# Optimization experiments

Measured on AMD Instinct MI355X. Metric: run time of the kernel, lower is better.

## Reference

```python
import jax, jax.numpy as jnp
import numpy as np

BATCH, SEQ, NUM_SUB, CB_SIZE, SUB_DIM = 8, 2048, 16, 1024, 64
EMB_DIM = NUM_SUB * SUB_DIM  # 1024


def setup_inputs() -> dict:
    key = jax.random.key(0)
    k1, k2 = jax.random.split(key)
    embeddings = jax.random.normal(k1, (BATCH, SEQ, EMB_DIM), dtype=jnp.float32)
    # stacked PQ codebooks: [num_subspaces, codebook_size, subspace_dim]
    codebooks = jax.random.normal(k2, (NUM_SUB, CB_SIZE, SUB_DIM), dtype=jnp.float32)
    return {"embeddings": embeddings, "codebooks": codebooks}


def reference(embeddings, codebooks):
    B, S, D = embeddings.shape
    M, K, d = codebooks.shape
    # [N, M, d] tokens split into subspaces
    x = embeddings.reshape(-1, M, d)
    x2 = jnp.sum(x * x, axis=-1, keepdims=True)            # [N, M, 1]
    c2 = jnp.sum(codebooks * codebooks, axis=-1)           # [M, K]
    xc = jnp.einsum('nmd,mkd->nmk', x, codebooks)          # [N, M, K]
    dist2 = x2 - 2.0 * xc + c2[None, :, :]
    indices = jnp.argmin(dist2, axis=-1)                   # [N, M] (argmin of sqdist == argmin of cdist)
    # gather nearest codeword per subspace: [N, M, d]
    quantized = jnp.take_along_axis(
        codebooks[None, :, :, :],                          # [1, M, K, d]
        indices[:, :, None, None],                         # [N, M, 1, 1]
        axis=2,
    )[:, :, 0, :]
    quantized = quantized.reshape(B, S, D)
    indices = indices.reshape(B, S, M).astype(jnp.int64)
    return quantized, indices
```

## Files before the change

kernel.cpp:

```cpp
#include <hip/hip_runtime.h>
#include <hip/hip_bf16.h>

#pragma clang fp contract(off)

#define NSUB 16
#define CBK  1024
#define SDIM 64
#define EMB  1024
#define NTOK 16384
#define TOKB 128
#define MARGIN 5e-3f

typedef __attribute__((ext_vector_type(8))) short bf16x8;
typedef __attribute__((ext_vector_type(4))) float f32x4;

__device__ __forceinline__ float fmul(float a, float b) { return __fmul_rn(a, b); }
__device__ __forceinline__ float fadd(float a, float b) { return __fadd_rn(a, b); }
__device__ __forceinline__ float fsub(float a, float b) { return __fsub_rn(a, b); }

__device__ __forceinline__ float np_sq64(const float* v) {
    float r[8];
    #pragma unroll
    for (int j = 0; j < 8; ++j) r[j] = fmul(v[j], v[j]);
    #pragma unroll
    for (int b = 1; b < 8; ++b) {
        #pragma unroll
        for (int j = 0; j < 8; ++j)
            r[j] = fadd(r[j], fmul(v[b * 8 + j], v[b * 8 + j]));
    }
    return fadd(fadd(fadd(r[0], r[1]), fadd(r[2], r[3])),
                fadd(fadd(r[4], r[5]), fadd(r[6], r[7])));
}

__device__ __forceinline__ void split_bf16(float v, short& hi, short& lo) {
    __hip_bfloat16 h = __float2bfloat16(v);
    float hf = __bfloat162float(h);
    __hip_bfloat16 e = __float2bfloat16(__fsub_rn(v, hf));
    hi = *(short*)&h;
    lo = *(short*)&e;
}

__global__ __launch_bounds__(256)
void prep_kernel(const float* __restrict__ cb,
                 unsigned short* __restrict__ bpack,
                 float* __restrict__ c2g)
{
    const int bx = blockIdx.x;
    const int m  = blockIdx.y;
    const int t  = threadIdx.x;
    const int w  = t >> 6, l = t & 63;
    const int tc = bx * 4 + w;
    const int cw = tc * 16 + (l & 15);
    const int dq = (l >> 4) * 8;

    #pragma unroll
    for (int c = 0; c < 2; ++c) {
        const float* src = cb + ((size_t)m * CBK + cw) * SDIM + c * 32 + dq;
        bf16x8 hv, lv;
        #pragma unroll
        for (int j = 0; j < 8; ++j) {
            short h, e; split_bf16(-2.0f * src[j], h, e);
            hv[j] = h; lv[j] = e;
        }
        size_t base = (((size_t)(m * 64 + tc) * 2 + c) * 2) * 512 + (size_t)l * 8;
        *(bf16x8*)(bpack + base)       = hv;
        *(bf16x8*)(bpack + base + 512) = lv;
    }
    if (t < 64) {
        const int row = bx * 64 + t;
        c2g[m * CBK + row] = np_sq64(cb + ((size_t)m * CBK + row) * SDIM);
    }
}

__global__ __launch_bounds__(256, 3)
void pq_mfma_kernel(const float* __restrict__ emb,
                    const float* __restrict__ cb,
                    const unsigned short* __restrict__ bpack,
                    const float* __restrict__ c2g,
                    float* __restrict__ qout,
                    float* __restrict__ iout)
{
    __shared__ float C2s[CBK];
    __shared__ float red_v[256];
    __shared__ int   red_k[256];
    __shared__ int   bestk_s[TOKB];
    __shared__ int   flag_s[TOKB];
    __shared__ int   cnt_s;

    const int m = blockIdx.y, tok0 = blockIdx.x * TOKB;
    const int t = threadIdx.x, w = t >> 6, l = t & 63;
    const int ln15 = l & 15, q = l >> 4;

    if (t == 0) cnt_s = 0;
    *(f32x4*)(C2s + t * 4) = *(const f32x4*)(c2g + m * CBK + t * 4);

    bf16x8 xh[2][2], xl[2][2];
    #pragma unroll
    for (int r = 0; r < 2; ++r) {
        const int tok = tok0 + w * 32 + r * 16 + ln15;
        #pragma unroll
        for (int c = 0; c < 2; ++c) {
            const float* src = emb + (size_t)tok * EMB + m * SDIM + c * 32 + q * 8;
            float4 v0 = *(const float4*)(src);
            float4 v1 = *(const float4*)(src + 4);
            float vv[8] = {v0.x,v0.y,v0.z,v0.w,v1.x,v1.y,v1.z,v1.w};
            #pragma unroll
            for (int j = 0; j < 8; ++j) {
                short h, e; split_bf16(vv[j], h, e);
                xh[r][c][j] = h; xl[r][c][j] = e;
            }
        }
    }
    __syncthreads();

    float v1t[2][4], v2t[2][4]; int k1t[2][4];
    #pragma unroll
    for (int r = 0; r < 2; ++r)
        #pragma unroll
        for (int g = 0; g < 4; ++g) { v1t[r][g] = 3.4e38f; v2t[r][g] = 3.4e38f; k1t[r][g] = 0; }

    const unsigned short* bptr = bpack + (size_t)m * 64 * 2048 + (size_t)l * 8;
    bf16x8 A0 = *(const bf16x8*)(bptr);
    bf16x8 A1 = *(const bf16x8*)(bptr + 512);
    bf16x8 A2 = *(const bf16x8*)(bptr + 1024);
    bf16x8 A3 = *(const bf16x8*)(bptr + 1536);

#define COMPUTE_TILE(B0, B1, B2, B3, TC)                                        \
    {                                                                           \
        const int kk = (TC) * 16 + ln15;                                        \
        const float c2v = C2s[kk];                                              \
        _Pragma("unroll")                                                       \
        for (int r = 0; r < 2; ++r) {                                           \
            f32x4 acc = {c2v, c2v, c2v, c2v};                                   \
            acc = __builtin_amdgcn_mfma_f32_16x16x32_bf16(xh[r][0], B0, acc, 0, 0, 0); \
            acc = __builtin_amdgcn_mfma_f32_16x16x32_bf16(xh[r][1], B2, acc, 0, 0, 0); \
            acc = __builtin_amdgcn_mfma_f32_16x16x32_bf16(xl[r][0], B0, acc, 0, 0, 0); \
            acc = __builtin_amdgcn_mfma_f32_16x16x32_bf16(xl[r][1], B2, acc, 0, 0, 0); \
            acc = __builtin_amdgcn_mfma_f32_16x16x32_bf16(xh[r][0], B1, acc, 0, 0, 0); \
            acc = __builtin_amdgcn_mfma_f32_16x16x32_bf16(xh[r][1], B3, acc, 0, 0, 0); \
            _Pragma("unroll")                                                   \
            for (int g = 0; g < 4; ++g) {                                       \
                float s = acc[g];                                               \
                v2t[r][g] = fminf(v2t[r][g], fmaxf(s, v1t[r][g]));              \
                bool lt = s < v1t[r][g];                                        \
                v1t[r][g] = lt ? s : v1t[r][g];                                 \
                k1t[r][g] = lt ? kk : k1t[r][g];                                \
            }                                                                   \
        }                                                                       \
    }

    for (int tc = 0; tc < 64; tc += 2) {
        const unsigned short* p1 = bptr + (size_t)(tc + 1) * 2048;
        bf16x8 N0 = *(const bf16x8*)(p1);
        bf16x8 N1 = *(const bf16x8*)(p1 + 512);
        bf16x8 N2 = *(const bf16x8*)(p1 + 1024);
        bf16x8 N3 = *(const bf16x8*)(p1 + 1536);
        COMPUTE_TILE(A0, A1, A2, A3, tc)
        if (tc + 2 < 64) {
            const unsigned short* p2 = bptr + (size_t)(tc + 2) * 2048;
            A0 = *(const bf16x8*)(p2);
            A1 = *(const bf16x8*)(p2 + 512);
            A2 = *(const bf16x8*)(p2 + 1024);
            A3 = *(const bf16x8*)(p2 + 1536);
        }
        COMPUTE_TILE(N0, N1, N2, N3, tc + 1)
    }
#undef COMPUTE_TILE
    __syncthreads();

    #pragma unroll
    for (int r = 0; r < 2; ++r) {
        #pragma unroll
        for (int g = 0; g < 4; ++g) {
            float v1 = v1t[r][g], v2 = v2t[r][g]; int k1 = k1t[r][g];
            #pragma unroll
            for (int mask = 1; mask < 16; mask <<= 1) {
                float ov1 = __shfl_xor(v1, mask);
                float ov2 = __shfl_xor(v2, mask);
                int   ok1 = __shfl_xor(k1, mask);
                if (ov1 < v1 || (ov1 == v1 && ok1 < k1)) {
                    v2 = fminf(v1, ov2);
                    v1 = ov1; k1 = ok1;
                } else {
                    v2 = fminf(v2, ov1);
                }
            }
            if (ln15 == 0) {
                const int token = w * 32 + r * 16 + q * 4 + g;
                if (v2 - v1 <= MARGIN) {
                    int slot = atomicAdd(&cnt_s, 1);
                    flag_s[slot] = token;
                } else {
                    bestk_s[token] = k1;
                    iout[(size_t)(tok0 + token) * NSUB + m] = (float)k1;
                }
            }
        }
    }
    __syncthreads();

    const int nflag = cnt_s;
    for (int f = 0; f < nflag; ++f) {
        const int token = flag_s[f];
        const float* xrow = emb + (size_t)(tok0 + token) * EMB + m * SDIM;
        const float x2v = np_sq64(xrow);
        float bs = 3.4e38f; int bk = CBK;
        #pragma unroll
        for (int rr = 0; rr < 4; ++rr) {
            const int k = t + 256 * rr;
            const float* crow = cb + ((size_t)m * CBK + k) * SDIM;
            float acc = 0.f;
            #pragma unroll
            for (int i = 0; i < 16; ++i) {
                float4 c4 = *(const float4*)(crow + 4 * i);
                float4 x4 = *(const float4*)(xrow + 4 * i);
                acc = __fmaf_rn(x4.x, c4.x, acc);
                acc = __fmaf_rn(x4.y, c4.y, acc);
                acc = __fmaf_rn(x4.z, c4.z, acc);
                acc = __fmaf_rn(x4.w, c4.w, acc);
            }
            const float dist = fadd(fsub(x2v, fmul(2.f, acc)), C2s[k]);
            if (dist < bs) { bs = dist; bk = k; }
        }
        red_v[t] = bs; red_k[t] = bk;
        __syncthreads();
        for (int off = 128; off > 0; off >>= 1) {
            if (t < off) {
                float o = red_v[t + off]; int ok = red_k[t + off];
                if (o < red_v[t] || (o == red_v[t] && ok < red_k[t])) {
                    red_v[t] = o; red_k[t] = ok;
                }
            }
            __syncthreads();
        }
        if (t == 0) {
            bestk_s[token] = red_k[0];
            iout[(size_t)(tok0 + token) * NSUB + m] = (float)red_k[0];
        }
        __syncthreads();
    }

    {
        const int tok = t >> 1, d0 = (t & 1) * 32;
        const int bk  = bestk_s[tok];
        const float* src = cb + ((size_t)m * CBK + bk) * SDIM + d0;
        float* dst = qout + (size_t)(tok0 + tok) * EMB + m * SDIM + d0;
        #pragma unroll
        for (int i = 0; i < 8; ++i)
            *(float4*)(dst + 4 * i) = *(const float4*)(src + 4 * i);
    }
}

extern "C" void kernel_launch(void* const* d_in, const int* in_sizes, int n_in,
                              void* d_out, int out_size, void* d_ws, size_t ws_size,
                              hipStream_t stream) {
    const float* emb = (const float*)d_in[0];
    const float* cb  = (const float*)d_in[1];
    float* qout = (float*)d_out;
    float* iout = (float*)d_out + (size_t)NTOK * EMB;

    unsigned short* bpack = (unsigned short*)d_ws;
    float* c2g = (float*)((char*)d_ws + 4u * 1024u * 1024u);

    prep_kernel<<<dim3(16, 16), 256, 0, stream>>>(cb, bpack, c2g);
    pq_mfma_kernel<<<dim3(NTOK / TOKB, NSUB), 256, 0, stream>>>(
        emb, cb, bpack, c2g, qout, iout);
}
```

Before: 288.5 us.

## Stage codebook tiles into LDS via async global_load_lds double buffering

The main kernel now copies packed bf16 codebook tiles into a double-buffered shared-memory array using direct global-to-LDS loads. Previously each wave read the same tiles from global memory into registers on its own. The loads for the next phase overlap with MFMA compute on the current one. It also raises the occupancy hint to 4 blocks per CU and gives the prep kernel twice as many blocks. The new 32KB LDS buffer and the per-phase barriers could limit occupancy or add synchronisation stalls.

```diff
diff --git a/kernel.cpp b/kernel.cpp
--- a/kernel.cpp
+++ b/kernel.cpp
@@ -38,6 +38,12 @@
     __hip_bfloat16 e = __float2bfloat16(__fsub_rn(v, hf));
     hi = *(short*)&h;
     lo = *(short*)&e;
+}
+
+typedef const __attribute__((address_space(1))) unsigned int gu32;
+typedef __attribute__((address_space(3))) unsigned int lu32;
+__device__ __forceinline__ void stage16(const void* g, void* l) {
+    __builtin_amdgcn_global_load_lds((gu32*)g, (lu32*)l, 16, 0, 0);
 }
 
 __global__ __launch_bounds__(256)
@@ -49,12 +55,12 @@
     const int m  = blockIdx.y;
     const int t  = threadIdx.x;
     const int w  = t >> 6, l = t & 63;
-    const int tc = bx * 4 + w;
+    const int tc = bx * 2 + (w & 1);
+    const int c  = w >> 1;
     const int cw = tc * 16 + (l & 15);
     const int dq = (l >> 4) * 8;
 
-    #pragma unroll
-    for (int c = 0; c < 2; ++c) {
+    {
         const float* src = cb + ((size_t)m * CBK + cw) * SDIM + c * 32 + dq;
         bf16x8 hv, lv;
         #pragma unroll
@@ -66,13 +72,13 @@
         *(bf16x8*)(bpack + base)       = hv;
         *(bf16x8*)(bpack + base + 512) = lv;
     }
-    if (t < 64) {
-        const int row = bx * 64 + t;
+    if (t < 32) {
+        const int row = bx * 32 + t;
         c2g[m * CBK + row] = np_sq64(cb + ((size_t)m * CBK + row) * SDIM);
     }
 }
 
-__global__ __launch_bounds__(256, 3)
+__global__ __launch_bounds__(256, 4)
 void pq_mfma_kernel(const float* __restrict__ emb,
                     const float* __restrict__ cb,
                     const unsigned short* __restrict__ bpack,
@@ -80,6 +86,7 @@
                     float* __restrict__ qout,
                     float* __restrict__ iout)
 {
+    __shared__ __align__(16) unsigned short bs[2][4 * 2048];
     __shared__ float C2s[CBK];
     __shared__ float red_v[256];
     __shared__ int   red_k[256];
@@ -94,6 +101,15 @@
     if (t == 0) cnt_s = 0;
     *(f32x4*)(C2s + t * 4) = *(const f32x4*)(c2g + m * CBK + t * 4);
 
+    const unsigned short* gB = bpack + (size_t)m * 64 * 2048;
+
+    {
+        const unsigned short* src = gB + t * 8;
+        #pragma unroll
+        for (int j = 0; j < 4; ++j)
+            stage16(src + j * 2048, &bs[0][j * 2048 + t * 8]);
+    }
+
     bf16x8 xh[2][2], xl[2][2];
     #pragma unroll
     for (int r = 0; r < 2; ++r) {
@@ -111,19 +127,14 @@
             }
         }
     }
+
+    float v1t[2][4], v2t[2][4]; int k1t[2][4];
+    #pragma unroll
+    for (int r = 0; r < 2; ++r)
+        #pragma unroll
+        for (int g = 0; g < 4; ++g) { v1t[r][g] = 3.4e38f; v2t[r][g] = 3.4e38f; k1t[r][g] = 0; }
+
     __syncthreads();
-
-    float v1t[2][4], v2t[2][4]; int k1t[2][4];
-    #pragma unroll
-    for (int r = 0; r < 2; ++r)
-        #pragma unroll
-        for (int g = 0; g < 4; ++g) { v1t[r][g] = 3.4e38f; v2t[r][g] = 3.4e38f; k1t[r][g] = 0; }
-
-    const unsigned short* bptr = bpack + (size_t)m * 64 * 2048 + (size_t)l * 8;
-    bf16x8 A0 = *(const bf16x8*)(bptr);
-    bf16x8 A1 = *(const bf16x8*)(bptr + 512);
-    bf16x8 A2 = *(const bf16x8*)(bptr + 1024);
-    bf16x8 A3 = *(const bf16x8*)(bptr + 1536);
 
 #define COMPUTE_TILE(B0, B1, B2, B3, TC)                                        \
     {                                                                           \
@@ -149,24 +160,27 @@
         }                                                                       \
     }
 
-    for (int tc = 0; tc < 64; tc += 2) {
-        const unsigned short* p1 = bptr + (size_t)(tc + 1) * 2048;
-        bf16x8 N0 = *(const bf16x8*)(p1);
-        bf16x8 N1 = *(const bf16x8*)(p1 + 512);
-        bf16x8 N2 = *(const bf16x8*)(p1 + 1024);
-        bf16x8 N3 = *(const bf16x8*)(p1 + 1536);
-        COMPUTE_TILE(A0, A1, A2, A3, tc)
-        if (tc + 2 < 64) {
-            const unsigned short* p2 = bptr + (size_t)(tc + 2) * 2048;
-            A0 = *(const bf16x8*)(p2);
-            A1 = *(const bf16x8*)(p2 + 512);
-            A2 = *(const bf16x8*)(p2 + 1024);
-            A3 = *(const bf16x8*)(p2 + 1536);
-        }
-        COMPUTE_TILE(N0, N1, N2, N3, tc + 1)
+    for (int ph = 0; ph < 16; ++ph) {
+        const int buf = ph & 1;
+        if (ph < 15) {
+            const unsigned short* src = gB + (size_t)(ph + 1) * 8192 + t * 8;
+            #pragma unroll
+            for (int j = 0; j < 4; ++j)
+                stage16(src + j * 2048, &bs[buf ^ 1][j * 2048 + t * 8]);
+        }
+        #pragma unroll
+        for (int j = 0; j < 4; ++j) {
+            const int tc = ph * 4 + j;
+            const unsigned short* bp = &bs[buf][j * 2048 + l * 8];
+            bf16x8 B0 = *(const bf16x8*)(bp);
+            bf16x8 B1 = *(const bf16x8*)(bp + 512);
+            bf16x8 B2 = *(const bf16x8*)(bp + 1024);
+            bf16x8 B3 = *(const bf16x8*)(bp + 1536);
+            COMPUTE_TILE(B0, B1, B2, B3, tc)
+        }
+        __syncthreads();
     }
 #undef COMPUTE_TILE
-    __syncthreads();
 
     #pragma unroll
     for (int r = 0; r < 2; ++r) {
@@ -204,7 +218,7 @@
         const int token = flag_s[f];
         const float* xrow = emb + (size_t)(tok0 + token) * EMB + m * SDIM;
         const float x2v = np_sq64(xrow);
-        float bs = 3.4e38f; int bk = CBK;
+        float bs_ = 3.4e38f; int bk = CBK;
         #pragma unroll
         for (int rr = 0; rr < 4; ++rr) {
             const int k = t + 256 * rr;
@@ -220,9 +234,9 @@
                 acc = __fmaf_rn(x4.w, c4.w, acc);
             }
             const float dist = fadd(fsub(x2v, fmul(2.f, acc)), C2s[k]);
-            if (dist < bs) { bs = dist; bk = k; }
-        }
-        red_v[t] = bs; red_k[t] = bk;
+            if (dist < bs_) { bs_ = dist; bk = k; }
+        }
+        red_v[t] = bs_; red_k[t] = bk;
         __syncthreads();
         for (int off = 128; off > 0; off >>= 1) {
             if (t < off) {
@@ -262,7 +276,7 @@
     unsigned short* bpack = (unsigned short*)d_ws;
     float* c2g = (float*)((char*)d_ws + 4u * 1024u * 1024u);
 
-    prep_kernel<<<dim3(16, 16), 256, 0, stream>>>(cb, bpack, c2g);
+    prep_kernel<<<dim3(32, 16), 256, 0, stream>>>(cb, bpack, c2g);
     pq_mfma_kernel<<<dim3(NTOK / TOKB, NSUB), 256, 0, stream>>>(
         emb, cb, bpack, c2g, qout, iout);
 }
```

Result: faster. 281.0 us (-2.6%).
